# Optimization experiments

Measured on AMD Instinct MI355X. Metric: run time of the kernel, lower is better.

Reference implementation:

```python
import jax, jax.numpy as jnp
import numpy as np

B, T, N_X, N_U, N_Y, H = 2048, 2048, 4, 2, 1, 64
MIN_X = jnp.array([0.0, 0.0, 0.0, -jnp.inf], dtype=jnp.float32)
MAX_X = jnp.array([10.0, 10.0, 10.0, jnp.inf], dtype=jnp.float32)
MIN_Y = jnp.array([0.0], dtype=jnp.float32)
MAX_Y = jnp.array([10.0], dtype=jnp.float32)


def setup_inputs() -> dict:
    key = jax.random.key(0)
    ks = jax.random.split(key, 6)
    return {
        "x_0": jax.random.uniform(ks[0], (B, N_X), dtype=jnp.float32) * 5.0,
        "u": jax.random.normal(ks[1], (B, T, N_U), dtype=jnp.float32),
        "theta_f": jnp.array([0.1925, 0.2429, 0.1697, 0.0444, 0.1642], dtype=jnp.float32),
        "theta_h": jnp.zeros((1,), dtype=jnp.float32),
        "tau_u": jnp.ones((1,), dtype=jnp.float32),
        "tau_y": jnp.ones((1,), dtype=jnp.float32),
        "W1": jax.random.normal(ks[2], (N_X + N_U + 5, H), dtype=jnp.float32) / np.sqrt(N_X + N_U + 5),
        "b1": jnp.zeros((H,), dtype=jnp.float32),
        "W2": jax.random.normal(ks[3], (H, N_X), dtype=jnp.float32) * 0.05,
        "Wh": jax.random.normal(ks[4], (N_X, N_Y), dtype=jnp.float32),
    }


def reference(x_0, u, theta_f, theta_h, tau_u, tau_y, W1, b1, W2, Wh):
    Bc = x_0.shape[0]
    tf = jnp.broadcast_to(theta_f[None, :], (Bc, theta_f.shape[0]))
    scale = tau_u[0] / tau_y[0]

    def f(x, ut):
        feat = jnp.concatenate([x, ut, tf], axis=-1)  # (B, n_x+n_u+5)
        return jnp.tanh(feat @ W1 + b1) @ W2 * scale  # (B, n_x)

    def h(x):
        return x @ Wh + theta_h  # (B, n_y)

    y0 = h(x_0)  # unclamped initial output, as in the torch loop

    def step(carry, ut):
        x_step, y_step = carry
        dx = f(x_step, ut)
        x_raw = x_step + dx
        y_new = jnp.clip(h(x_raw), MIN_Y, MAX_Y)  # y computed from pre-clamp state
        x_new = jnp.clip(x_raw, MIN_X, MAX_X)
        return (x_new, y_new), (x_step, y_step)

    u_t = jnp.moveaxis(u, 1, 0)  # (T, B, n_u)
    _, (xs, ys) = jax.lax.scan(step, (x_0, y0), u_t)
    x = jnp.moveaxis(xs, 0, 1)  # (B, T, n_x)
    y = jnp.moveaxis(ys, 0, 1)  # (B, T, n_y)
    return (x, y)
```

## Files before the change

kernel.cpp:

```cpp
#include <hip/hip_runtime.h>

#define B_SZ 2048
#define T_SZ 2048

using f32x16 = float __attribute__((ext_vector_type(16)));

template<int CTRL>
__device__ __forceinline__ float dppf(float v) {
  int r = __builtin_amdgcn_update_dpp(0, __builtin_bit_cast(int, v), CTRL, 0xf, 0xf, true);
  return __builtin_bit_cast(float, r);
}

__device__ __forceinline__ float swz16(float v) {
  return __builtin_bit_cast(float,
      __builtin_amdgcn_ds_swizzle(__builtin_bit_cast(int, v), 0x401F));
}

__device__ __forceinline__ float bperm(int addr_bytes, float v) {
  return __builtin_bit_cast(float,
      __builtin_amdgcn_ds_bpermute(addr_bytes, __builtin_bit_cast(int, v)));
}

__global__ __launch_bounds__(256, 2) void sss_kernel(
    const float* __restrict__ x0p, const float* __restrict__ up,
    const float* __restrict__ tfp, const float* __restrict__ thp,
    const float* __restrict__ tup, const float* __restrict__ typ,
    const float* __restrict__ W1p, const float* __restrict__ b1p,
    const float* __restrict__ W2p, const float* __restrict__ Whp,
    float* __restrict__ outp)
{
  const int lane = threadIdx.x & 63;
  const int wv   = __builtin_amdgcn_readfirstlane((int)(threadIdx.x >> 6));
  const int b    = blockIdx.x * 4 + wv;

  const float K = 2.8853900817779268f;
  const float w1x0 = W1p[0 * 64 + lane] * K;
  const float w1x1 = W1p[1 * 64 + lane] * K;
  const float w1x2 = W1p[2 * 64 + lane] * K;
  const float w1x3 = W1p[3 * 64 + lane] * K;
  const float w1u0 = W1p[4 * 64 + lane] * K;
  const float w1u1 = W1p[5 * 64 + lane] * K;

  float cc = b1p[lane];
#pragma unroll
  for (int j = 0; j < 5; ++j)
    cc = fmaf(tfp[j], W1p[(6 + j) * 64 + lane], cc);
  cc *= K;

  const float scale = tup[0] / typ[0];
  const float4 w2r = ((const float4*)W2p)[lane];
  const float w2_0 = w2r.x * scale;
  const float w2_1 = w2r.y * scale;
  const float w2_2 = w2r.z * scale;
  const float w2_3 = w2r.w * scale;
  const bool lb0 = lane & 1;
  const bool lb1 = (lane >> 1) & 1;
  const float w2A = lb0 ? w2_1 : w2_0;
  const float w2B = lb0 ? w2_0 : w2_1;
  const float w2C = lb0 ? w2_3 : w2_2;
  const float w2D = lb0 ? w2_2 : w2_3;

  const float whl = Whp[lane & 3];
  const float th  = thp[0];

  const float lo = ((lane & 3) == 3) ? -__builtin_inff() : 0.0f;
  const float hi = ((lane & 3) == 3) ?  __builtin_inff() : 10.0f;

  float xlane = x0p[b * 4 + (lane & 3)];
  float x0v = dppf<0x00>(xlane);
  float x1v = dppf<0x55>(xlane);
  float x2v = dppf<0xAA>(xlane);
  float x3v = dppf<0xFF>(xlane);

  float p0 = xlane * whl;
  p0 += dppf<0xB1>(p0);
  p0 += dppf<0x4E>(p0);
  float yv = p0 + th;

  unsigned voff, vinc;
  if (lane < 4) {
    voff = (unsigned)(b * (T_SZ * 4) + lane) * 4u;
    vinc = 16u;
  } else {
    voff = (unsigned)((unsigned)B_SZ * T_SZ * 4u + (unsigned)b * T_SZ) * 4u;
    vinc = (lane == 4) ? 4u : 0u;
  }
  const bool doSt = (lane < 5);
  const bool is4  = (lane == 4);

  const int addr32 = (lane ^ 32) << 2;
  const int addr48 = (lane ^ 48) << 2;

  const f32x16* up16 = (const f32x16*)(up + (size_t)b * (T_SZ * 2));
  char* outB = (char*)outp;

  f32x16 uch = up16[0];
  const int NC = T_SZ / 8;

  for (int c = 0; c < NC; ++c) {
    const int g = (c + 1 < NC) ? c + 1 : NC - 1;
    const f32x16 unx = up16[g];
#pragma unroll
    for (int j = 0; j < 8; ++j) {
      const float vdata = is4 ? yv : xlane;
      if (doSt) *(float*)(outB + voff) = vdata;
      voff += vinc;

      const float u0 = uch[2 * j];
      const float u1 = uch[2 * j + 1];

      float a0 = fmaf(u0, w1u0, cc);
      a0 = fmaf(x0v, w1x0, a0);
      a0 = fmaf(x2v, w1x2, a0);
      float a1 = u1 * w1u1;
      a1 = fmaf(x1v, w1x1, a1);
      a1 = fmaf(x3v, w1x3, a1);
      const float acc = a0 + a1;

      const float e  = __builtin_amdgcn_exp2f(acc);
      const float rr = __builtin_amdgcn_rcpf(e + 1.0f);
      const float h  = fmaf(-2.0f, rr, 1.0f);

      const float pA = h * w2A, pB = h * w2B, pC = h * w2C, pD = h * w2D;
      const float r0 = pA + dppf<0xB1>(pB);
      const float r1 = pC + dppf<0xB1>(pD);
      const float keep = lb1 ? r1 : r0;
      const float send = lb1 ? r0 : r1;
      float v = keep + dppf<0x4E>(send);
      v += dppf<0x124>(v);
      v += dppf<0x128>(v);
      const float a16 = swz16(v);
      const float a32 = bperm(addr32, v);
      const float a48 = bperm(addr48, v);
      v = (v + a16) + (a32 + a48);

      const float w = xlane + v;
      xlane = __builtin_amdgcn_fmed3f(w, lo, hi);

      float p = w * whl;
      p += dppf<0xB1>(p);
      p += dppf<0x4E>(p);
      yv = __builtin_amdgcn_fmed3f(p + th, 0.0f, 10.0f);

      x0v = dppf<0x00>(xlane);
      x1v = dppf<0x55>(xlane);
      x2v = dppf<0xAA>(xlane);
      x3v = dppf<0xFF>(xlane);
    }
    uch = unx;
  }
}

extern "C" void kernel_launch(void* const* d_in, const int* in_sizes, int n_in,
                              void* d_out, int out_size, void* d_ws, size_t ws_size,
                              hipStream_t stream) {
  (void)in_sizes; (void)n_in; (void)out_size; (void)d_ws; (void)ws_size;
  sss_kernel<<<dim3(B_SZ / 4), dim3(256), 0, stream>>>(
      (const float*)d_in[0], (const float*)d_in[1], (const float*)d_in[2],
      (const float*)d_in[3], (const float*)d_in[4], (const float*)d_in[5],
      (const float*)d_in[6], (const float*)d_in[7], (const float*)d_in[8],
      (const float*)d_in[9], (float*)d_out);
}
```

Measured before the change: 389.5 us.

## Pack two batch rows per wavefront with 32 lanes each handling two hidden units

```diff
diff --git a/kernel.cpp b/kernel.cpp
--- a/kernel.cpp
+++ b/kernel.cpp
@@ -16,12 +16,7 @@
       __builtin_amdgcn_ds_swizzle(__builtin_bit_cast(int, v), 0x401F));
 }
 
-__device__ __forceinline__ float bperm(int addr_bytes, float v) {
-  return __builtin_bit_cast(float,
-      __builtin_amdgcn_ds_bpermute(addr_bytes, __builtin_bit_cast(int, v)));
-}
-
-__global__ __launch_bounds__(256, 2) void sss_kernel(
+__global__ __launch_bounds__(256) void sss_kernel(
     const float* __restrict__ x0p, const float* __restrict__ up,
     const float* __restrict__ tfp, const float* __restrict__ thp,
     const float* __restrict__ tup, const float* __restrict__ typ,
@@ -31,34 +26,40 @@
 {
   const int lane = threadIdx.x & 63;
   const int wv   = __builtin_amdgcn_readfirstlane((int)(threadIdx.x >> 6));
-  const int b    = blockIdx.x * 4 + wv;
+  const int half = lane >> 5;
+  const int j    = lane & 31;
+  const int b    = blockIdx.x * 8 + wv * 2 + half;
 
   const float K = 2.8853900817779268f;
-  const float w1x0 = W1p[0 * 64 + lane] * K;
-  const float w1x1 = W1p[1 * 64 + lane] * K;
-  const float w1x2 = W1p[2 * 64 + lane] * K;
-  const float w1x3 = W1p[3 * 64 + lane] * K;
-  const float w1u0 = W1p[4 * 64 + lane] * K;
-  const float w1u1 = W1p[5 * 64 + lane] * K;
-
-  float cc = b1p[lane];
+  float w1a[6], w1b[6];
 #pragma unroll
-  for (int j = 0; j < 5; ++j)
-    cc = fmaf(tfp[j], W1p[(6 + j) * 64 + lane], cc);
-  cc *= K;
+  for (int c = 0; c < 6; ++c) {
+    w1a[c] = W1p[c * 64 + j]      * K;
+    w1b[c] = W1p[c * 64 + j + 32] * K;
+  }
+  float cca = b1p[j], ccb = b1p[j + 32];
+#pragma unroll
+  for (int q = 0; q < 5; ++q) {
+    cca = fmaf(tfp[q], W1p[(6 + q) * 64 + j],      cca);
+    ccb = fmaf(tfp[q], W1p[(6 + q) * 64 + j + 32], ccb);
+  }
+  cca *= K; ccb *= K;
 
   const float scale = tup[0] / typ[0];
-  const float4 w2r = ((const float4*)W2p)[lane];
-  const float w2_0 = w2r.x * scale;
-  const float w2_1 = w2r.y * scale;
-  const float w2_2 = w2r.z * scale;
-  const float w2_3 = w2r.w * scale;
+  const float4 wra = ((const float4*)W2p)[j];
+  const float4 wrb = ((const float4*)W2p)[j + 32];
+  const float sa0 = wra.x * scale, sa1 = wra.y * scale, sa2 = wra.z * scale, sa3 = wra.w * scale;
+  const float sb0 = wrb.x * scale, sb1 = wrb.y * scale, sb2 = wrb.z * scale, sb3 = wrb.w * scale;
   const bool lb0 = lane & 1;
   const bool lb1 = (lane >> 1) & 1;
-  const float w2A = lb0 ? w2_1 : w2_0;
-  const float w2B = lb0 ? w2_0 : w2_1;
-  const float w2C = lb0 ? w2_3 : w2_2;
-  const float w2D = lb0 ? w2_2 : w2_3;
+  const float w2Aa = lb0 ? sa1 : sa0;
+  const float w2Ba = lb0 ? sa0 : sa1;
+  const float w2Ca = lb0 ? sa3 : sa2;
+  const float w2Da = lb0 ? sa2 : sa3;
+  const float w2Ab = lb0 ? sb1 : sb0;
+  const float w2Bb = lb0 ? sb0 : sb1;
+  const float w2Cb = lb0 ? sb3 : sb2;
+  const float w2Db = lb0 ? sb2 : sb3;
 
   const float whl = Whp[lane & 3];
   const float th  = thp[0];
@@ -77,19 +78,17 @@
   p0 += dppf<0x4E>(p0);
   float yv = p0 + th;
 
+  const int sl = lane & 31;
   unsigned voff, vinc;
-  if (lane < 4) {
-    voff = (unsigned)(b * (T_SZ * 4) + lane) * 4u;
+  if (sl < 4) {
+    voff = (unsigned)(b * (T_SZ * 4) + sl) * 4u;
     vinc = 16u;
   } else {
     voff = (unsigned)((unsigned)B_SZ * T_SZ * 4u + (unsigned)b * T_SZ) * 4u;
-    vinc = (lane == 4) ? 4u : 0u;
+    vinc = (sl == 4) ? 4u : 0u;
   }
-  const bool doSt = (lane < 5);
-  const bool is4  = (lane == 4);
-
-  const int addr32 = (lane ^ 32) << 2;
-  const int addr48 = (lane ^ 48) << 2;
+  const bool doSt = (sl < 5);
+  const bool is4  = (sl == 4);
 
   const f32x16* up16 = (const f32x16*)(up + (size_t)b * (T_SZ * 2));
   char* outB = (char*)outp;
@@ -101,38 +100,49 @@
     const int g = (c + 1 < NC) ? c + 1 : NC - 1;
     const f32x16 unx = up16[g];
 #pragma unroll
-    for (int j = 0; j < 8; ++j) {
+    for (int jj = 0; jj < 8; ++jj) {
       const float vdata = is4 ? yv : xlane;
       if (doSt) *(float*)(outB + voff) = vdata;
       voff += vinc;
 
-      const float u0 = uch[2 * j];
-      const float u1 = uch[2 * j + 1];
+      const float u0 = uch[2 * jj];
+      const float u1 = uch[2 * jj + 1];
 
-      float a0 = fmaf(u0, w1u0, cc);
-      a0 = fmaf(x0v, w1x0, a0);
-      a0 = fmaf(x2v, w1x2, a0);
-      float a1 = u1 * w1u1;
-      a1 = fmaf(x1v, w1x1, a1);
-      a1 = fmaf(x3v, w1x3, a1);
-      const float acc = a0 + a1;
+      float a0 = fmaf(u0, w1a[4], cca);
+      a0 = fmaf(x0v, w1a[0], a0);
+      a0 = fmaf(x2v, w1a[2], a0);
+      float a1 = u1 * w1a[5];
+      a1 = fmaf(x1v, w1a[1], a1);
+      a1 = fmaf(x3v, w1a[3], a1);
+      const float acca = a0 + a1;
 
-      const float e  = __builtin_amdgcn_exp2f(acc);
-      const float rr = __builtin_amdgcn_rcpf(e + 1.0f);
-      const float h  = fmaf(-2.0f, rr, 1.0f);
+      float b0 = fmaf(u0, w1b[4], ccb);
+      b0 = fmaf(x0v, w1b[0], b0);
+      b0 = fmaf(x2v, w1b[2], b0);
+      float b1 = u1 * w1b[5];
+      b1 = fmaf(x1v, w1b[1], b1);
+      b1 = fmaf(x3v, w1b[3], b1);
+      const float accb = b0 + b1;
 
-      const float pA = h * w2A, pB = h * w2B, pC = h * w2C, pD = h * w2D;
-      const float r0 = pA + dppf<0xB1>(pB);
-      const float r1 = pC + dppf<0xB1>(pD);
+      const float ea = __builtin_amdgcn_exp2f(acca);
+      const float ra = __builtin_amdgcn_rcpf(ea + 1.0f);
+      const float ha = fmaf(-2.0f, ra, 1.0f);
+      const float eb = __builtin_amdgcn_exp2f(accb);
+      const float rb = __builtin_amdgcn_rcpf(eb + 1.0f);
+      const float hb = fmaf(-2.0f, rb, 1.0f);
+
+      const float qA = fmaf(hb, w2Ab, ha * w2Aa);
+      const float qB = fmaf(hb, w2Bb, ha * w2Ba);
+      const float qC = fmaf(hb, w2Cb, ha * w2Ca);
+      const float qD = fmaf(hb, w2Db, ha * w2Da);
+      const float r0 = qA + dppf<0xB1>(qB);
+      const float r1 = qC + dppf<0xB1>(qD);
       const float keep = lb1 ? r1 : r0;
       const float send = lb1 ? r0 : r1;
       float v = keep + dppf<0x4E>(send);
       v += dppf<0x124>(v);
       v += dppf<0x128>(v);
-      const float a16 = swz16(v);
-      const float a32 = bperm(addr32, v);
-      const float a48 = bperm(addr48, v);
-      v = (v + a16) + (a32 + a48);
+      v += swz16(v);
 
       const float w = xlane + v;
       xlane = __builtin_amdgcn_fmed3f(w, lo, hi);
@@ -155,7 +165,7 @@
                               void* d_out, int out_size, void* d_ws, size_t ws_size,
                               hipStream_t stream) {
   (void)in_sizes; (void)n_in; (void)out_size; (void)d_ws; (void)ws_size;
-  sss_kernel<<<dim3(B_SZ / 4), dim3(256), 0, stream>>>(
+  sss_kernel<<<dim3(B_SZ / 8), dim3(256), 0, stream>>>(
       (const float*)d_in[0], (const float*)d_in[1], (const float*)d_in[2],
       (const float*)d_in[3], (const float*)d_in[4], (const float*)d_in[5],
       (const float*)d_in[6], (const float*)d_in[7], (const float*)d_in[8],
```

New measurement: 370.1 us. -5.0%, faster.

## Compute four hidden units per lane to keep the W2 reduction within one row

Applied to the files above, without the earlier changes.

```diff
diff --git a/kernel.cpp b/kernel.cpp
--- a/kernel.cpp
+++ b/kernel.cpp
@@ -11,17 +11,7 @@
   return __builtin_bit_cast(float, r);
 }
 
-__device__ __forceinline__ float swz16(float v) {
-  return __builtin_bit_cast(float,
-      __builtin_amdgcn_ds_swizzle(__builtin_bit_cast(int, v), 0x401F));
-}
-
-__device__ __forceinline__ float bperm(int addr_bytes, float v) {
-  return __builtin_bit_cast(float,
-      __builtin_amdgcn_ds_bpermute(addr_bytes, __builtin_bit_cast(int, v)));
-}
-
-__global__ __launch_bounds__(256, 2) void sss_kernel(
+__global__ __launch_bounds__(256) void sss_kernel(
     const float* __restrict__ x0p, const float* __restrict__ up,
     const float* __restrict__ tfp, const float* __restrict__ thp,
     const float* __restrict__ tup, const float* __restrict__ typ,
@@ -32,41 +22,44 @@
   const int lane = threadIdx.x & 63;
   const int wv   = __builtin_amdgcn_readfirstlane((int)(threadIdx.x >> 6));
   const int b    = blockIdx.x * 4 + wv;
+  const int sl   = lane & 15;
+  const int k    = lane & 3;
 
   const float K = 2.8853900817779268f;
-  const float w1x0 = W1p[0 * 64 + lane] * K;
-  const float w1x1 = W1p[1 * 64 + lane] * K;
-  const float w1x2 = W1p[2 * 64 + lane] * K;
-  const float w1x3 = W1p[3 * 64 + lane] * K;
-  const float w1u0 = W1p[4 * 64 + lane] * K;
-  const float w1u1 = W1p[5 * 64 + lane] * K;
-
-  float cc = b1p[lane];
+  float w1[4][6], cc[4];
 #pragma unroll
-  for (int j = 0; j < 5; ++j)
-    cc = fmaf(tfp[j], W1p[(6 + j) * 64 + lane], cc);
-  cc *= K;
+  for (int c = 0; c < 4; ++c) {
+    const int u = sl + 16 * c;
+#pragma unroll
+    for (int r = 0; r < 6; ++r) w1[c][r] = W1p[r * 64 + u] * K;
+    float t = b1p[u];
+#pragma unroll
+    for (int q = 0; q < 5; ++q) t = fmaf(tfp[q], W1p[(6 + q) * 64 + u], t);
+    cc[c] = t * K;
+  }
 
   const float scale = tup[0] / typ[0];
-  const float4 w2r = ((const float4*)W2p)[lane];
-  const float w2_0 = w2r.x * scale;
-  const float w2_1 = w2r.y * scale;
-  const float w2_2 = w2r.z * scale;
-  const float w2_3 = w2r.w * scale;
-  const bool lb0 = lane & 1;
-  const bool lb1 = (lane >> 1) & 1;
-  const float w2A = lb0 ? w2_1 : w2_0;
-  const float w2B = lb0 ? w2_0 : w2_1;
-  const float w2C = lb0 ? w2_3 : w2_2;
-  const float w2D = lb0 ? w2_2 : w2_3;
+  float wA[4], wB[4], wC[4], wD[4];
+#pragma unroll
+  for (int c = 0; c < 4; ++c) {
+    const int u = sl + 16 * c;
+    const float4 w2r = ((const float4*)W2p)[u];
+    const float s0 = w2r.x * scale, s1 = w2r.y * scale;
+    const float s2 = w2r.z * scale, s3 = w2r.w * scale;
+    float col[4] = {s0, s1, s2, s3};
+    wA[c] = col[k];
+    wB[c] = col[k ^ 1];
+    wC[c] = col[k ^ 2];
+    wD[c] = col[k ^ 3];
+  }
 
-  const float whl = Whp[lane & 3];
+  const float whl = Whp[k];
   const float th  = thp[0];
 
-  const float lo = ((lane & 3) == 3) ? -__builtin_inff() : 0.0f;
-  const float hi = ((lane & 3) == 3) ?  __builtin_inff() : 10.0f;
+  const float lo = (k == 3) ? -__builtin_inff() : 0.0f;
+  const float hi = (k == 3) ?  __builtin_inff() : 10.0f;
 
-  float xlane = x0p[b * 4 + (lane & 3)];
+  float xlane = x0p[b * 4 + k];
   float x0v = dppf<0x00>(xlane);
   float x1v = dppf<0x55>(xlane);
   float x2v = dppf<0xAA>(xlane);
@@ -88,9 +81,6 @@
   const bool doSt = (lane < 5);
   const bool is4  = (lane == 4);
 
-  const int addr32 = (lane ^ 32) << 2;
-  const int addr48 = (lane ^ 48) << 2;
-
   const f32x16* up16 = (const f32x16*)(up + (size_t)b * (T_SZ * 2));
   char* outB = (char*)outp;
 
@@ -101,38 +91,40 @@
     const int g = (c + 1 < NC) ? c + 1 : NC - 1;
     const f32x16 unx = up16[g];
 #pragma unroll
-    for (int j = 0; j < 8; ++j) {
+    for (int jj = 0; jj < 8; ++jj) {
       const float vdata = is4 ? yv : xlane;
       if (doSt) *(float*)(outB + voff) = vdata;
       voff += vinc;
 
-      const float u0 = uch[2 * j];
-      const float u1 = uch[2 * j + 1];
+      const float u0 = uch[2 * jj];
+      const float u1 = uch[2 * jj + 1];
 
-      float a0 = fmaf(u0, w1u0, cc);
-      a0 = fmaf(x0v, w1x0, a0);
-      a0 = fmaf(x2v, w1x2, a0);
-      float a1 = u1 * w1u1;
-      a1 = fmaf(x1v, w1x1, a1);
-      a1 = fmaf(x3v, w1x3, a1);
-      const float acc = a0 + a1;
+      float base[4];
+#pragma unroll
+      for (int cu = 0; cu < 4; ++cu)
+        base[cu] = fmaf(u1, w1[cu][5], fmaf(u0, w1[cu][4], cc[cu]));
 
-      const float e  = __builtin_amdgcn_exp2f(acc);
-      const float rr = __builtin_amdgcn_rcpf(e + 1.0f);
-      const float h  = fmaf(-2.0f, rr, 1.0f);
+      float h[4];
+#pragma unroll
+      for (int cu = 0; cu < 4; ++cu) {
+        const float m01 = fmaf(x1v, w1[cu][1], x0v * w1[cu][0]);
+        const float m23 = fmaf(x3v, w1[cu][3], x2v * w1[cu][2]);
+        const float acc = (base[cu] + m01) + m23;
+        const float e  = __builtin_amdgcn_exp2f(acc);
+        const float rr = __builtin_amdgcn_rcpf(e + 1.0f);
+        h[cu] = fmaf(-2.0f, rr, 1.0f);
+      }
 
-      const float pA = h * w2A, pB = h * w2B, pC = h * w2C, pD = h * w2D;
-      const float r0 = pA + dppf<0xB1>(pB);
-      const float r1 = pC + dppf<0xB1>(pD);
-      const float keep = lb1 ? r1 : r0;
-      const float send = lb1 ? r0 : r1;
-      float v = keep + dppf<0x4E>(send);
+      const float qA = fmaf(h[1], wA[1], h[0] * wA[0]) + fmaf(h[3], wA[3], h[2] * wA[2]);
+      const float qB = fmaf(h[1], wB[1], h[0] * wB[0]) + fmaf(h[3], wB[3], h[2] * wB[2]);
+      const float qC = fmaf(h[1], wC[1], h[0] * wC[0]) + fmaf(h[3], wC[3], h[2] * wC[2]);
+      const float qD = fmaf(h[1], wD[1], h[0] * wD[0]) + fmaf(h[3], wD[3], h[2] * wD[2]);
+
+      const float r0 = qA + dppf<0xB1>(qB);
+      const float r1 = qC + dppf<0xB1>(qD);
+      float v = r0 + dppf<0x4E>(r1);
       v += dppf<0x124>(v);
       v += dppf<0x128>(v);
-      const float a16 = swz16(v);
-      const float a32 = bperm(addr32, v);
-      const float a48 = bperm(addr48, v);
-      v = (v + a16) + (a32 + a48);
 
       const float w = xlane + v;
       xlane = __builtin_amdgcn_fmed3f(w, lo, hi);
```

New measurement: 659.9 us. 69.4% more time.
